# Kernel optimization log

Measured on AMD Instinct MI355X. Metric: run time of the kernel, lower is better.

The kernel has to match this reference:

```python
import jax, jax.numpy as jnp
import numpy as np

N_NODES = 50000
N_EDGES = 800000
N_GRAPHS = 512
IN_F = 128
HEADS = 8
HEAD_C = 8
OUT_F = HEADS * HEAD_C  # 64
NEG_SLOPE = 0.2


def setup_inputs() -> dict:
    key = jax.random.key(0)
    ks = jax.random.split(key, 10)
    x = jax.random.normal(ks[0], (N_NODES, IN_F), dtype=jnp.float32)
    edge_index = jax.random.randint(ks[1], (2, N_EDGES), 0, N_NODES, dtype=jnp.int64)
    batch = jnp.sort(jax.random.randint(ks[2], (N_NODES,), 0, N_GRAPHS, dtype=jnp.int64))
    s = 0.05
    W = jax.random.normal(ks[3], (IN_F, OUT_F), dtype=jnp.float32) * s
    att_src = jax.random.normal(ks[4], (HEADS, HEAD_C), dtype=jnp.float32) * s
    att_dst = jax.random.normal(ks[5], (HEADS, HEAD_C), dtype=jnp.float32) * s
    bias = jax.random.normal(ks[6], (OUT_F,), dtype=jnp.float32) * s
    pool_w_rel = jax.random.normal(ks[7], (OUT_F, 1), dtype=jnp.float32) * s
    pool_b_rel = jax.random.normal(ks[8], (1,), dtype=jnp.float32) * s
    pool_w_root = jax.random.normal(ks[9], (OUT_F, 1), dtype=jnp.float32) * s
    return {"x": x, "edge_index": edge_index, "batch": batch, "W": W,
            "att_src": att_src, "att_dst": att_dst, "bias": bias,
            "pool_w_rel": pool_w_rel, "pool_b_rel": pool_b_rel,
            "pool_w_root": pool_w_root}


def _segment_softmax(e, seg, num_segments):
    # numerically stable scatter-softmax over segments
    m = jax.ops.segment_max(e, seg, num_segments=num_segments)
    ex = jnp.exp(e - m[seg])
    denom = jax.ops.segment_sum(ex, seg, num_segments=num_segments)
    return ex / (denom[seg] + 1e-16)


def reference(x, edge_index, batch, W, att_src, att_dst, bias,
              pool_w_rel, pool_b_rel, pool_w_root):
    N = N_NODES
    # ---- GATConv (concat heads, self-loops added, LeakyReLU 0.2) ----
    loops = jnp.arange(N, dtype=edge_index.dtype)
    src = jnp.concatenate([edge_index[0], loops])
    dst = jnp.concatenate([edge_index[1], loops])
    h = (x @ W).reshape(N, HEADS, HEAD_C)                 # [N,H,C]
    a_s = jnp.einsum('nhc,hc->nh', h, att_src)            # [N,H]
    a_d = jnp.einsum('nhc,hc->nh', h, att_dst)
    e = jax.nn.leaky_relu(a_s[src] + a_d[dst], NEG_SLOPE) # [E+N,H]
    alpha = _segment_softmax(e, dst, N)                   # softmax over incoming edges
    out = jax.ops.segment_sum(h[src] * alpha[:, :, None], dst, num_segments=N)
    out = out.reshape(N, OUT_F) + bias                    # [N,64]
    # ---- SAGPooling(min_score=-1): GraphConv score + per-graph softmax,
    #      all nodes kept (softmax scores > -1), features scaled by score ----
    s2, d2 = edge_index[0], edge_index[1]
    aggr = jax.ops.segment_sum(out[s2], d2, num_segments=N)  # add-aggregation
    score = (aggr @ pool_w_rel + pool_b_rel + out @ pool_w_root)[:, 0]  # [N]
    score = _segment_softmax(score, batch, N_GRAPHS)
    att_x = out * score[:, None]
    # ---- global_add_pool ----
    g = jax.ops.segment_sum(att_x, batch, num_segments=N_GRAPHS)  # [G,64]
    return out, g
```

## Files before the change

### kernel.cpp

```cpp
#include <hip/hip_runtime.h>

#define NN 50000
#define NE 800000
#define NG 512
#define INF_ 128
#define OUTF 64
#define CAP 64

#define NPART 4
#define PSIZE 12500
#define NCHUNK 250
#define CHUNKE 3200

#define GEMM_BLOCKS ((NN + 63) / 64)
#define FRONT_BLOCKS (NCHUNK * 8)

#define XSTRIDE 136

__device__ __forceinline__ unsigned short f2bf(float f) {
    unsigned int u = __float_as_uint(f);
    unsigned int r = (u + 0x7fffu + ((u >> 16) & 1u)) >> 16;
    return (unsigned short)r;
}
__device__ __forceinline__ float bf2f(unsigned int lo16) {
    return __uint_as_float(lo16 << 16);
}

__global__ __launch_bounds__(256) void k_front(
    const int* __restrict__ ei, int* __restrict__ deg,
    unsigned short* __restrict__ adj, float* __restrict__ gden,
    float* __restrict__ g_num,
    const float* __restrict__ x, const float* __restrict__ W,
    const float* __restrict__ att_src, const float* __restrict__ att_dst,
    unsigned short* __restrict__ hb, float* __restrict__ a_s,
    float* __restrict__ a_d)
{
    __shared__ float Ws[INF_ * OUTF];
    __shared__ unsigned short Xs[64 * XSTRIDE];

    const int r   = blockIdx.x & 7;
    const int oct = blockIdx.x >> 3;

    if (r < NPART) {
        const int adj_id = oct * NPART + r;
        {
            int idx = adj_id * 256 + threadIdx.x;
            if (idx < NG) gden[idx] = 0.f;
            else if (idx < NG + NG * OUTF) g_num[idx - NG] = 0.f;
        }
        const int lo = r * PSIZE;
        const int e0 = oct * CHUNKE;
        const int e1 = (e0 + CHUNKE < NE) ? e0 + CHUNKE : NE;
        for (int e = e0 + threadIdx.x; e < e1; e += 256) {
            int d = ei[NE + e];
            unsigned int rel = (unsigned int)(d - lo);
            if (rel < PSIZE) {
                int s = ei[e];
                int p = atomicAdd(&deg[d], 1);
                if (p < CAP) adj[(size_t)d * CAP + p] = (unsigned short)s;
            }
        }
        return;
    }

    const int bid = oct * 4 + (r - 4);
    if (bid >= GEMM_BLOCKS) return;
    const int n0 = bid * 64;

    for (int i = threadIdx.x; i < INF_ * OUTF / 4; i += 256)
        ((float4*)Ws)[i] = ((const float4*)W)[i];

    #pragma unroll
    for (int it = 0; it < 8; it++) {
        int idx = it * 256 + threadIdx.x;
        int row = idx >> 5;
        int c4  = idx & 31;
        int n = n0 + row;
        if (n > NN - 1) n = NN - 1;
        float4 v = ((const float4*)(x + (size_t)n * INF_))[c4];
        ushort4 b;
        b.x = f2bf(v.x); b.y = f2bf(v.y); b.z = f2bf(v.z); b.w = f2bf(v.w);
        *(ushort4*)&Xs[row * XSTRIDE + c4 * 4] = b;
    }
    __syncthreads();

    const int colg = threadIdx.x & 15;
    const int rowg = threadIdx.x >> 4;

    const unsigned short* xr[4];
    #pragma unroll
    for (int rr = 0; rr < 4; rr++)
        xr[rr] = &Xs[(rowg * 4 + rr) * XSTRIDE];

    float acc[4][4];
    #pragma unroll
    for (int rr = 0; rr < 4; rr++)
        #pragma unroll
        for (int c = 0; c < 4; c++) acc[rr][c] = 0.f;

    for (int k8 = 0; k8 < INF_ / 8; k8++) {
        uint4 xv[4];
        #pragma unroll
        for (int rr = 0; rr < 4; rr++)
            xv[rr] = *(const uint4*)(xr[rr] + k8 * 8);
        #pragma unroll
        for (int kk = 0; kk < 8; kk++) {
            float4 wv = ((const float4*)&Ws[(k8 * 8 + kk) * OUTF])[colg];
            #pragma unroll
            for (int rr = 0; rr < 4; rr++) {
                unsigned int pair = ((const unsigned int*)&xv[rr])[kk >> 1];
                float xs_ = bf2f((kk & 1) ? (pair >> 16) : (pair & 0xffffu));
                acc[rr][0] = fmaf(xs_, wv.x, acc[rr][0]);
                acc[rr][1] = fmaf(xs_, wv.y, acc[rr][1]);
                acc[rr][2] = fmaf(xs_, wv.z, acc[rr][2]);
                acc[rr][3] = fmaf(xs_, wv.w, acc[rr][3]);
            }
        }
    }

    float asv[4], adv[4];
    #pragma unroll
    for (int c = 0; c < 4; c++) {
        asv[c] = att_src[colg * 4 + c];
        adv[c] = att_dst[colg * 4 + c];
    }

    #pragma unroll
    for (int rr = 0; rr < 4; rr++) {
        const int n = n0 + rowg * 4 + rr;
        const bool valid = (n < NN);
        if (valid) {
            ushort4 o;
            o.x = f2bf(acc[rr][0]); o.y = f2bf(acc[rr][1]);
            o.z = f2bf(acc[rr][2]); o.w = f2bf(acc[rr][3]);
            ((ushort4*)(hb + (size_t)n * OUTF))[colg] = o;
        }
        float vs = acc[rr][0]*asv[0] + acc[rr][1]*asv[1] + acc[rr][2]*asv[2] + acc[rr][3]*asv[3];
        float vd = acc[rr][0]*adv[0] + acc[rr][1]*adv[1] + acc[rr][2]*adv[2] + acc[rr][3]*adv[3];
        vs += __shfl_xor(vs, 1, 64);
        vd += __shfl_xor(vd, 1, 64);
        if (valid && !(colg & 1)) {
            a_s[n * 8 + (colg >> 1)] = vs;
            a_d[n * 8 + (colg >> 1)] = vd;
        }
    }
}

__global__ __launch_bounds__(256) void k_aggr(
    const unsigned short* __restrict__ hb, const float* __restrict__ a_s,
    const float* __restrict__ a_d, const int* __restrict__ deg,
    const unsigned short* __restrict__ adj, const float* __restrict__ bias,
    const float* __restrict__ w_rel, const float* __restrict__ w_root,
    float* __restrict__ out, float* __restrict__ t_rel, float* __restrict__ t_root)
{
    const int wid  = threadIdx.x >> 6;
    const int lane = threadIdx.x & 63;
    const int g    = lane >> 3;
    const int c8   = lane & 7;
    const int n    = blockIdx.x * 4 + wid;
    if (n >= NN) return;

    const float ad_n = a_d[n * 8 + c8];

    float acc[8];
    #pragma unroll
    for (int k = 0; k < 8; k++) acc[k] = 0.f;
    float den = 0.f;

    if (g == 0) {
        float e0 = a_s[n * 8 + c8] + ad_n;
        e0 = e0 > 0.f ? e0 : 0.2f * e0;
        float ex0 = __expf(e0);
        uint4 hv = *(const uint4*)(hb + (size_t)n * OUTF + c8 * 8);
        acc[0] = ex0 * bf2f(hv.x & 0xffffu); acc[1] = ex0 * bf2f(hv.x >> 16);
        acc[2] = ex0 * bf2f(hv.y & 0xffffu); acc[3] = ex0 * bf2f(hv.y >> 16);
        acc[4] = ex0 * bf2f(hv.z & 0xffffu); acc[5] = ex0 * bf2f(hv.z >> 16);
        acc[6] = ex0 * bf2f(hv.w & 0xffffu); acc[7] = ex0 * bf2f(hv.w >> 16);
        den = ex0;
    }

    const int cnt = min(deg[n], CAP);
    const unsigned short* lst = adj + (size_t)n * CAP;
    for (int i = g; i < cnt; i += 8) {
        int s = lst[i];
        float as = a_s[s * 8 + c8];
        uint4 hv = *(const uint4*)(hb + (size_t)s * OUTF + c8 * 8);
        float e = as + ad_n;
        e = e > 0.f ? e : 0.2f * e;
        float ex = __expf(e);
        acc[0] = fmaf(ex, bf2f(hv.x & 0xffffu), acc[0]);
        acc[1] = fmaf(ex, bf2f(hv.x >> 16),     acc[1]);
        acc[2] = fmaf(ex, bf2f(hv.y & 0xffffu), acc[2]);
        acc[3] = fmaf(ex, bf2f(hv.y >> 16),     acc[3]);
        acc[4] = fmaf(ex, bf2f(hv.z & 0xffffu), acc[4]);
        acc[5] = fmaf(ex, bf2f(hv.z >> 16),     acc[5]);
        acc[6] = fmaf(ex, bf2f(hv.w & 0xffffu), acc[6]);
        acc[7] = fmaf(ex, bf2f(hv.w >> 16),     acc[7]);
        den += ex;
    }

    #pragma unroll
    for (int m = 8; m < 64; m <<= 1) {
        den += __shfl_xor(den, m, 64);
        #pragma unroll
        for (int k = 0; k < 8; k++) acc[k] += __shfl_xor(acc[k], m, 64);
    }

    const float inv = 1.f / (den + 1e-16f);
    float o[8];
    #pragma unroll
    for (int k = 0; k < 8; k++) o[k] = acc[k] * inv + bias[c8 * 8 + k];

    if (g == 0) {
        float4 o0 = make_float4(o[0], o[1], o[2], o[3]);
        float4 o1 = make_float4(o[4], o[5], o[6], o[7]);
        float4* op = (float4*)(out + (size_t)n * OUTF + c8 * 8);
        op[0] = o0; op[1] = o1;
    }

    float vr = 0.f, vt = 0.f;
    #pragma unroll
    for (int k = 0; k < 8; k++) {
        vr = fmaf(o[k], w_rel[c8 * 8 + k], vr);
        vt = fmaf(o[k], w_root[c8 * 8 + k], vt);
    }
    #pragma unroll
    for (int m = 1; m < 8; m <<= 1) {
        vr += __shfl_xor(vr, m, 64);
        vt += __shfl_xor(vt, m, 64);
    }
    if (lane == 0) { t_rel[n] = vr; t_root[n] = vt; }
}

__global__ __launch_bounds__(256) void k_score_pool(
    const int* __restrict__ deg, const unsigned short* __restrict__ adj,
    const float* __restrict__ t_rel, const float* __restrict__ t_root,
    const float* __restrict__ pool_b, const int* __restrict__ batch,
    const float* __restrict__ out,
    float* __restrict__ gden, float* __restrict__ g_num)
{
    __shared__ float ex_s[32];
    __shared__ int   b_s[32];

    const int wid  = threadIdx.x >> 6;
    const int lane = threadIdx.x & 63;
    const int sub  = lane >> 3;
    const int g    = lane & 7;
    const int base_n = blockIdx.x * 32;
    const int n    = base_n + wid * 8 + sub;

    const int cnt = (n < NN) ? min(deg[n], CAP) : 0;
    const unsigned short* lst = adj + (size_t)n * CAP;
    float acc = 0.f;
    for (int i = g; i < cnt; i += 8) acc += t_rel[lst[i]];
    #pragma unroll
    for (int m = 1; m < 8; m <<= 1) acc += __shfl_xor(acc, m, 64);

    if (g == 0) {
        const int slot = wid * 8 + sub;
        if (n < NN) {
            float ex = __expf(acc + t_root[n] + pool_b[0]);
            ex_s[slot] = ex;
            b_s[slot]  = batch[n];
        } else {
            ex_s[slot] = 0.f;
            b_s[slot]  = -1;
        }
    }
    __syncthreads();

    if (threadIdx.x == 0) {
        float racc = 0.f;
        int bcur = -1;
        for (int i = 0; i < 32; i++) {
            int b = b_s[i];
            if (b != bcur) {
                if (bcur >= 0) atomicAdd(&gden[bcur], racc);
                bcur = b; racc = 0.f;
            }
            racc += ex_s[i];
        }
        if (bcur >= 0) atomicAdd(&gden[bcur], racc);
    }

    const int j = lane;
    float facc = 0.f;
    int bcur = -1;
    for (int i = 0; i < 8; i++) {
        const int slot = wid * 8 + i;
        const int n2 = base_n + slot;
        if (n2 >= NN) break;
        int b = b_s[slot];
        if (b != bcur) {
            if (bcur >= 0) atomicAdd(&g_num[bcur * OUTF + j], facc);
            bcur = b; facc = 0.f;
        }
        facc = fmaf(out[(size_t)n2 * OUTF + j], ex_s[slot], facc);
    }
    if (bcur >= 0) atomicAdd(&g_num[bcur * OUTF + j], facc);
}

__global__ __launch_bounds__(256) void k_gfinal(
    const float* __restrict__ g_num, const float* __restrict__ gden,
    float* __restrict__ g)
{
    int i = blockIdx.x * 256 + threadIdx.x;
    if (i < NG * OUTF) g[i] = g_num[i] / (gden[i >> 6] + 1e-16f);
}

extern "C" void kernel_launch(void* const* d_in, const int* in_sizes, int n_in,
                              void* d_out, int out_size, void* d_ws, size_t ws_size,
                              hipStream_t stream)
{
    const float* x        = (const float*)d_in[0];
    const int*   ei       = (const int*)  d_in[1];
    const int*   batch    = (const int*)  d_in[2];
    const float* W        = (const float*)d_in[3];
    const float* att_src  = (const float*)d_in[4];
    const float* att_dst  = (const float*)d_in[5];
    const float* bias     = (const float*)d_in[6];
    const float* w_rel    = (const float*)d_in[7];
    const float* pool_b   = (const float*)d_in[8];
    const float* w_root   = (const float*)d_in[9];

    float* out_nodes = (float*)d_out;
    float* g_out     = (float*)d_out + (size_t)NN * OUTF;

    char* base = (char*)d_ws;
    unsigned short* hb = (unsigned short*)(base);
    float* a_s       = (float*)(base +  6400000);
    float* a_d       = (float*)(base +  8000000);
    float* t_rel     = (float*)(base +  9600000);
    float* t_root    = (float*)(base +  9800000);
    float* gden      = (float*)(base + 10000000);
    float* g_num     = (float*)(base + 10002048);
    int*   deg       = (int*)  (base + 10133120);
    unsigned short* adjl = (unsigned short*)(base + 10333120);

    hipMemsetAsync(deg, 0, (size_t)NN * 4, stream);

    k_front<<<FRONT_BLOCKS, 256, 0, stream>>>(
        ei, deg, adjl, gden, g_num,
        x, W, att_src, att_dst, hb, a_s, a_d);
    k_aggr<<<(NN + 3) / 4, 256, 0, stream>>>(hb, a_s, a_d, deg, adjl, bias,
                                             w_rel, w_root, out_nodes, t_rel, t_root);
    k_score_pool<<<(NN + 31) / 32, 256, 0, stream>>>(deg, adjl, t_rel, t_root,
                                                     pool_b, batch, out_nodes,
                                                     gden, g_num);
    k_gfinal<<<(NG * OUTF + 255) / 256, 256, 0, stream>>>(g_num, gden, g_out);
}
```

Before: 181.4 us.

## Use persistent work-stealing blocks with XCD-aware destination partitions in front kernel

Replaces the static interleaving of adjacency-build blocks and GEMM blocks with a persistent grid where every block pulls work from global atomic counters. It first drains edge chunks for each of 8 destination partitions, starting with the partition matching its XCC_ID so atomics on deg stay local to one XCD's L2, then pulls GEMM row tiles. Counters are zeroed by the existing memset. This is meant to balance load and improve atomic locality, but adds counter contention, extra block barriers, and depends on the XCC_ID register read.

```diff
diff --git a/kernel.cpp b/kernel.cpp
--- a/kernel.cpp
+++ b/kernel.cpp
@@ -7,13 +7,13 @@
 #define OUTF 64
 #define CAP 64
 
-#define NPART 4
-#define PSIZE 12500
+#define NPART 8
+#define PSIZE 6250
 #define NCHUNK 250
 #define CHUNKE 3200
 
 #define GEMM_BLOCKS ((NN + 63) / 64)
-#define FRONT_BLOCKS (NCHUNK * 8)
+#define FRONT_BLOCKS 2782
 
 #define XSTRIDE 136
 
@@ -29,7 +29,7 @@
 __global__ __launch_bounds__(256) void k_front(
     const int* __restrict__ ei, int* __restrict__ deg,
     unsigned short* __restrict__ adj, float* __restrict__ gden,
-    float* __restrict__ g_num,
+    float* __restrict__ g_num, int* __restrict__ ctrs,
     const float* __restrict__ x, const float* __restrict__ W,
     const float* __restrict__ att_src, const float* __restrict__ att_dst,
     unsigned short* __restrict__ hb, float* __restrict__ a_s,
@@ -37,87 +37,46 @@
 {
     __shared__ float Ws[INF_ * OUTF];
     __shared__ unsigned short Xs[64 * XSTRIDE];
-
-    const int r   = blockIdx.x & 7;
-    const int oct = blockIdx.x >> 3;
-
-    if (r < NPART) {
-        const int adj_id = oct * NPART + r;
-        {
-            int idx = adj_id * 256 + threadIdx.x;
-            if (idx < NG) gden[idx] = 0.f;
-            else if (idx < NG + NG * OUTF) g_num[idx - NG] = 0.f;
-        }
-        const int lo = r * PSIZE;
-        const int e0 = oct * CHUNKE;
-        const int e1 = (e0 + CHUNKE < NE) ? e0 + CHUNKE : NE;
-        for (int e = e0 + threadIdx.x; e < e1; e += 256) {
-            int d = ei[NE + e];
-            unsigned int rel = (unsigned int)(d - lo);
-            if (rel < PSIZE) {
-                int s = ei[e];
-                int p = atomicAdd(&deg[d], 1);
-                if (p < CAP) adj[(size_t)d * CAP + p] = (unsigned short)s;
-            }
-        }
-        return;
-    }
-
-    const int bid = oct * 4 + (r - 4);
-    if (bid >= GEMM_BLOCKS) return;
-    const int n0 = bid * 64;
+    __shared__ int s_work;
+
+    {
+        int idx = blockIdx.x * 256 + threadIdx.x;
+        if (idx < NG) gden[idx] = 0.f;
+        else if (idx < NG + NG * OUTF) g_num[idx - NG] = 0.f;
+    }
+
+    unsigned int xcd;
+    asm volatile("s_getreg_b32 %0, hwreg(HW_REG_XCC_ID)" : "=s"(xcd));
+    xcd &= 7;
+
+    for (int off = 0; off < NPART; off++) {
+        const int p  = (xcd + off) & (NPART - 1);
+        const int lo = p * PSIZE;
+        for (;;) {
+            __syncthreads();
+            if (threadIdx.x == 0) s_work = atomicAdd(&ctrs[p], 1);
+            __syncthreads();
+            const int c = s_work;
+            if (c >= NCHUNK) break;
+            const int e0 = c * CHUNKE;
+            const int e1 = (e0 + CHUNKE < NE) ? e0 + CHUNKE : NE;
+            for (int e = e0 + threadIdx.x; e < e1; e += 256) {
+                int d = ei[NE + e];
+                unsigned int rel = (unsigned int)(d - lo);
+                if (rel < PSIZE) {
+                    int s = ei[e];
+                    int pos = atomicAdd(&deg[d], 1);
+                    if (pos < CAP) adj[(size_t)d * CAP + pos] = (unsigned short)s;
+                }
+            }
+        }
+    }
 
     for (int i = threadIdx.x; i < INF_ * OUTF / 4; i += 256)
         ((float4*)Ws)[i] = ((const float4*)W)[i];
 
-    #pragma unroll
-    for (int it = 0; it < 8; it++) {
-        int idx = it * 256 + threadIdx.x;
-        int row = idx >> 5;
-        int c4  = idx & 31;
-        int n = n0 + row;
-        if (n > NN - 1) n = NN - 1;
-        float4 v = ((const float4*)(x + (size_t)n * INF_))[c4];
-        ushort4 b;
-        b.x = f2bf(v.x); b.y = f2bf(v.y); b.z = f2bf(v.z); b.w = f2bf(v.w);
-        *(ushort4*)&Xs[row * XSTRIDE + c4 * 4] = b;
-    }
-    __syncthreads();
-
     const int colg = threadIdx.x & 15;
     const int rowg = threadIdx.x >> 4;
-
-    const unsigned short* xr[4];
-    #pragma unroll
-    for (int rr = 0; rr < 4; rr++)
-        xr[rr] = &Xs[(rowg * 4 + rr) * XSTRIDE];
-
-    float acc[4][4];
-    #pragma unroll
-    for (int rr = 0; rr < 4; rr++)
-        #pragma unroll
-        for (int c = 0; c < 4; c++) acc[rr][c] = 0.f;
-
-    for (int k8 = 0; k8 < INF_ / 8; k8++) {
-        uint4 xv[4];
-        #pragma unroll
-        for (int rr = 0; rr < 4; rr++)
-            xv[rr] = *(const uint4*)(xr[rr] + k8 * 8);
-        #pragma unroll
-        for (int kk = 0; kk < 8; kk++) {
-            float4 wv = ((const float4*)&Ws[(k8 * 8 + kk) * OUTF])[colg];
-            #pragma unroll
-            for (int rr = 0; rr < 4; rr++) {
-                unsigned int pair = ((const unsigned int*)&xv[rr])[kk >> 1];
-                float xs_ = bf2f((kk & 1) ? (pair >> 16) : (pair & 0xffffu));
-                acc[rr][0] = fmaf(xs_, wv.x, acc[rr][0]);
-                acc[rr][1] = fmaf(xs_, wv.y, acc[rr][1]);
-                acc[rr][2] = fmaf(xs_, wv.z, acc[rr][2]);
-                acc[rr][3] = fmaf(xs_, wv.w, acc[rr][3]);
-            }
-        }
-    }
-
     float asv[4], adv[4];
     #pragma unroll
     for (int c = 0; c < 4; c++) {
@@ -125,23 +84,77 @@
         adv[c] = att_dst[colg * 4 + c];
     }
 
-    #pragma unroll
-    for (int rr = 0; rr < 4; rr++) {
-        const int n = n0 + rowg * 4 + rr;
-        const bool valid = (n < NN);
-        if (valid) {
-            ushort4 o;
-            o.x = f2bf(acc[rr][0]); o.y = f2bf(acc[rr][1]);
-            o.z = f2bf(acc[rr][2]); o.w = f2bf(acc[rr][3]);
-            ((ushort4*)(hb + (size_t)n * OUTF))[colg] = o;
-        }
-        float vs = acc[rr][0]*asv[0] + acc[rr][1]*asv[1] + acc[rr][2]*asv[2] + acc[rr][3]*asv[3];
-        float vd = acc[rr][0]*adv[0] + acc[rr][1]*adv[1] + acc[rr][2]*adv[2] + acc[rr][3]*adv[3];
-        vs += __shfl_xor(vs, 1, 64);
-        vd += __shfl_xor(vd, 1, 64);
-        if (valid && !(colg & 1)) {
-            a_s[n * 8 + (colg >> 1)] = vs;
-            a_d[n * 8 + (colg >> 1)] = vd;
+    for (;;) {
+        __syncthreads();
+        if (threadIdx.x == 0) s_work = atomicAdd(&ctrs[NPART], 1);
+        __syncthreads();
+        const int bid = s_work;
+        if (bid >= GEMM_BLOCKS) break;
+        const int n0 = bid * 64;
+
+        #pragma unroll
+        for (int it = 0; it < 8; it++) {
+            int idx = it * 256 + threadIdx.x;
+            int row = idx >> 5;
+            int c4  = idx & 31;
+            int n = n0 + row;
+            if (n > NN - 1) n = NN - 1;
+            float4 v = ((const float4*)(x + (size_t)n * INF_))[c4];
+            ushort4 b;
+            b.x = f2bf(v.x); b.y = f2bf(v.y); b.z = f2bf(v.z); b.w = f2bf(v.w);
+            *(ushort4*)&Xs[row * XSTRIDE + c4 * 4] = b;
+        }
+        __syncthreads();
+
+        const unsigned short* xr[4];
+        #pragma unroll
+        for (int rr = 0; rr < 4; rr++)
+            xr[rr] = &Xs[(rowg * 4 + rr) * XSTRIDE];
+
+        float acc[4][4];
+        #pragma unroll
+        for (int rr = 0; rr < 4; rr++)
+            #pragma unroll
+            for (int c = 0; c < 4; c++) acc[rr][c] = 0.f;
+
+        for (int k8 = 0; k8 < INF_ / 8; k8++) {
+            uint4 xv[4];
+            #pragma unroll
+            for (int rr = 0; rr < 4; rr++)
+                xv[rr] = *(const uint4*)(xr[rr] + k8 * 8);
+            #pragma unroll
+            for (int kk = 0; kk < 8; kk++) {
+                float4 wv = ((const float4*)&Ws[(k8 * 8 + kk) * OUTF])[colg];
+                #pragma unroll
+                for (int rr = 0; rr < 4; rr++) {
+                    unsigned int pair = ((const unsigned int*)&xv[rr])[kk >> 1];
+                    float xs_ = bf2f((kk & 1) ? (pair >> 16) : (pair & 0xffffu));
+                    acc[rr][0] = fmaf(xs_, wv.x, acc[rr][0]);
+                    acc[rr][1] = fmaf(xs_, wv.y, acc[rr][1]);
+                    acc[rr][2] = fmaf(xs_, wv.z, acc[rr][2]);
+                    acc[rr][3] = fmaf(xs_, wv.w, acc[rr][3]);
+                }
+            }
+        }
+
+        #pragma unroll
+        for (int rr = 0; rr < 4; rr++) {
+            const int n = n0 + rowg * 4 + rr;
+            const bool valid = (n < NN);
+            if (valid) {
+                ushort4 o;
+                o.x = f2bf(acc[rr][0]); o.y = f2bf(acc[rr][1]);
+                o.z = f2bf(acc[rr][2]); o.w = f2bf(acc[rr][3]);
+                ((ushort4*)(hb + (size_t)n * OUTF))[colg] = o;
+            }
+            float vs = acc[rr][0]*asv[0] + acc[rr][1]*asv[1] + acc[rr][2]*asv[2] + acc[rr][3]*asv[3];
+            float vd = acc[rr][0]*adv[0] + acc[rr][1]*adv[1] + acc[rr][2]*adv[2] + acc[rr][3]*adv[3];
+            vs += __shfl_xor(vs, 1, 64);
+            vd += __shfl_xor(vd, 1, 64);
+            if (valid && !(colg & 1)) {
+                a_s[n * 8 + (colg >> 1)] = vs;
+                a_d[n * 8 + (colg >> 1)] = vd;
+            }
         }
     }
 }
@@ -335,12 +348,13 @@
     float* gden      = (float*)(base + 10000000);
     float* g_num     = (float*)(base + 10002048);
     int*   deg       = (int*)  (base + 10133120);
-    unsigned short* adjl = (unsigned short*)(base + 10333120);
-
-    hipMemsetAsync(deg, 0, (size_t)NN * 4, stream);
+    int*   ctrs     = (int*)   (base + 10333120);
+    unsigned short* adjl = (unsigned short*)(base + 10333184);
+
+    hipMemsetAsync(deg, 0, (size_t)NN * 4 + 64, stream);
 
     k_front<<<FRONT_BLOCKS, 256, 0, stream>>>(
-        ei, deg, adjl, gden, g_num,
+        ei, deg, adjl, gden, g_num, ctrs,
         x, W, att_src, att_dst, hb, a_s, a_d);
     k_aggr<<<(NN + 3) / 4, 256, 0, stream>>>(hb, a_s, a_d, deg, adjl, bias,
                                              w_rel, w_root, out_nodes, t_rel, t_root);
```

Measured after the change: 475.8 us. 2.62x slower.
